# Optimization experiments

Hardware: AMD Instinct MI355X
Metric: run time of the kernel (lower is better)

Reference implementation:

```python
import jax, jax.numpy as jnp
import numpy as np

B, S, DIM = 1, 2048, 4096
N_HEADS, N_KV_HEADS = 32, 8
HEAD_DIM = DIM // N_HEADS            # 128
N_REP = N_HEADS // N_KV_HEADS        # 4
Q_SIZE = N_HEADS * HEAD_DIM          # 4096
KV_SIZE = N_KV_HEADS * HEAD_DIM      # 1024


def setup_inputs() -> dict:
    key = jax.random.key(0)
    ks = jax.random.split(key, 5)
    x = jax.random.normal(ks[0], (B, S, DIM), dtype=jnp.float32)
    # RoPE tables: freqs_cis[s, j] = exp(i * s * theta_j), theta_j = 10000^(-2j/head_dim)
    theta = 10000.0 ** (-jnp.arange(0, HEAD_DIM, 2, dtype=jnp.float32) / HEAD_DIM)
    ang = jnp.arange(S, dtype=jnp.float32)[:, None] * theta[None, :]  # [S, HEAD_DIM//2]
    freqs_cos = jnp.cos(ang)
    freqs_sin = jnp.sin(ang)
    # causal additive mask [1,1,S,S]
    causal = jnp.tril(jnp.ones((S, S), dtype=bool))
    mask = jnp.where(causal, 0.0, -1e9).astype(jnp.float32)[None, None]
    wqkv = jax.random.normal(ks[1], (Q_SIZE + 2 * KV_SIZE, DIM), dtype=jnp.float32) * (DIM ** -0.5)
    wo = jax.random.normal(ks[2], (DIM, Q_SIZE), dtype=jnp.float32) * (Q_SIZE ** -0.5)
    return {"x": x, "freqs_cos": freqs_cos, "freqs_sin": freqs_sin, "mask": mask,
            "wqkv": wqkv, "wo": wo}


def _apply_rope(t, cos, sin):
    # t: [B, S, H, D]; cos/sin: [S, D//2]  (complex multiply on (even, odd) pairs)
    b, s, h, d = t.shape
    tp = t.reshape(b, s, h, d // 2, 2)
    t0, t1 = tp[..., 0], tp[..., 1]
    c = cos[None, :, None, :]
    sn = sin[None, :, None, :]
    out = jnp.stack([t0 * c - t1 * sn, t0 * sn + t1 * c], axis=-1)
    return out.reshape(b, s, h, d)


def reference(x, freqs_cos, freqs_sin, mask, wqkv, wo):
    bsz, seqlen, _ = x.shape
    qkv = jnp.einsum('bsd,od->bso', x, wqkv)  # fused QKV projection
    xq = qkv[..., :Q_SIZE].reshape(bsz, seqlen, N_HEADS, HEAD_DIM)
    xk = qkv[..., Q_SIZE:Q_SIZE + KV_SIZE].reshape(bsz, seqlen, N_KV_HEADS, HEAD_DIM)
    xv = qkv[..., Q_SIZE + KV_SIZE:].reshape(bsz, seqlen, N_KV_HEADS, HEAD_DIM)
    # rotary embedding on q, k
    xq = _apply_rope(xq, freqs_cos, freqs_sin)
    xk = _apply_rope(xk, freqs_cos, freqs_sin)
    # cache insertion (prefill: cache == current k/v), layout [B, KVH, S, D]
    cache_k = jnp.swapaxes(xk, 1, 2)
    cache_v = jnp.swapaxes(xv, 1, 2)
    # GQA repeat_kv -> [B, H, S, D]
    keys = jnp.repeat(cache_k, N_REP, axis=1)
    values = jnp.repeat(cache_v, N_REP, axis=1)
    # scores: einsum 'ijkl,ikml->ikjm' with xq [b,s,h,d], keys [b,h,t,d] -> [b,h,s,t]
    scores = jnp.einsum('bshd,bhtd->bhst', xq, keys) / jnp.sqrt(jnp.float32(HEAD_DIM))
    scores = scores + mask
    scores = jax.nn.softmax(scores.astype(jnp.float32), axis=-1).astype(xq.dtype)
    out = jnp.einsum('bhst,bhtd->bhsd', scores, values)  # [B, H, S, D]
    out = jnp.swapaxes(out, 1, 2).reshape(bsz, seqlen, Q_SIZE)
    return jnp.einsum('bso,do->bsd', out, wo)
```

## Files before the change

kernel.cpp:

```cpp
#include <hip/hip_runtime.h>
#include <hip/hip_bf16.h>
#include <cstdint>
#include <cstddef>


typedef __attribute__((ext_vector_type(4)))  float    f32x4;
typedef __attribute__((ext_vector_type(16))) float    f32x16;
typedef __attribute__((ext_vector_type(8)))  __bf16   bf16x8;
typedef __attribute__((ext_vector_type(4)))  __bf16   bf16x4;
typedef __attribute__((ext_vector_type(2)))  __bf16   bf16x2;
typedef __attribute__((ext_vector_type(4)))  uint32_t u32x4;

typedef const __attribute__((address_space(1))) void* gaddr_t;
typedef __attribute__((address_space(3))) void*       laddr_t;

#define S_LEN   2048
#define DIM_    4096
#define NHEADS  32
#define NKV     8
#define HD      128
#define QKV_LD  6144
#define KOFF    4096
#define VOFF    5120

#define EXP2F(x) __builtin_amdgcn_exp2f(x)

#define N4_X  2097152
#define N4_W  6291456
#define N4_O  4194304
__global__ void cvt3(const float* __restrict__ x, __bf16* __restrict__ xb,
                     const float* __restrict__ wq, __bf16* __restrict__ wqb,
                     const float* __restrict__ wo, __bf16* __restrict__ wob) {
  int idx = blockIdx.x * blockDim.x + threadIdx.x;
  int stride = gridDim.x * blockDim.x;
  for (int i = idx; i < N4_X + N4_W + N4_O; i += stride) {
    const float* src; __bf16* dst; int k;
    if (i < N4_X)            { src = x;  dst = xb;  k = i; }
    else if (i < N4_X + N4_W){ src = wq; dst = wqb; k = i - N4_X; }
    else                     { src = wo; dst = wob; k = i - N4_X - N4_W; }
    float4 v = reinterpret_cast<const float4*>(src)[k];
    bf16x4 o;
    o[0] = (__bf16)v.x; o[1] = (__bf16)v.y; o[2] = (__bf16)v.z; o[3] = (__bf16)v.w;
    reinterpret_cast<bf16x4*>(dst)[k] = o;
  }
}

__global__ void rope_kernel(__bf16* __restrict__ qkv, const float* __restrict__ fc,
                            const float* __restrict__ fs) {
  int tid = blockIdx.x * 256 + threadIdx.x;
  int i = tid & 63;
  int t = tid >> 6;
  int h = t % 40;
  int s = t / 40;
  int col = (h < NHEADS) ? (h * HD + 2 * i) : (KOFF + (h - NHEADS) * HD + 2 * i);
  size_t off = (size_t)s * QKV_LD + col;
  float c = fc[s * 64 + i], sn = fs[s * 64 + i];
  bf16x2 v = *reinterpret_cast<bf16x2*>(&qkv[off]);
  float t0 = (float)v[0], t1 = (float)v[1];
  bf16x2 o;
  o[0] = (__bf16)(t0 * c - t1 * sn);
  o[1] = (__bf16)(t0 * sn + t1 * c);
  *reinterpret_cast<bf16x2*>(&qkv[off]) = o;
}

__device__ __forceinline__ void stg64(const __bf16* __restrict__ P, int ld, int row0,
                                      int kt, char* dst, int tid) {
  int r = tid >> 3, g = tid & 7;
  int row = row0 + r;
  const __bf16* src = P + (size_t)row * ld + kt * 64 + ((g ^ (row & 7)) * 8);
  __builtin_amdgcn_global_load_lds((gaddr_t)src,
      (laddr_t)(dst + (tid & ~63) * 16), 16, 0, 0);
}

template <int QM, int QN, bool RA, bool RB, int VW>
__device__ __forceinline__ void g1_phase(const __bf16* __restrict__ Ab,
                                         const __bf16* __restrict__ Bb,
                                         f32x4 (&acc)[8][4],
                                         bf16x8 (&afr)[4][2], bf16x8 (&bfr)[2][2],
                                         int wm, int wn, int l15, int hi, int tid,
                                         const __bf16* __restrict__ SP, int sld,
                                         int srow, int skt, char* sdst, bool doSt) {
  if constexpr (RA) {
#pragma unroll
    for (int fm = 0; fm < 4; ++fm) {
      int R = wm * 128 + QM * 64 + fm * 16 + l15;
#pragma unroll
      for (int kk = 0; kk < 2; ++kk)
        afr[fm][kk] = *reinterpret_cast<const bf16x8*>(
            (const char*)Ab + R * 128 + (((kk * 4 + hi) ^ (R & 7)) * 16));
    }
  }
  if constexpr (RB) {
#pragma unroll
    for (int fn = 0; fn < 2; ++fn) {
      int R = wn * 64 + QN * 32 + fn * 16 + l15;
#pragma unroll
      for (int kk = 0; kk < 2; ++kk)
        bfr[fn][kk] = *reinterpret_cast<const bf16x8*>(
            (const char*)Bb + R * 128 + (((kk * 4 + hi) ^ (R & 7)) * 16));
    }
  }
  if (doSt) {
    stg64(SP, sld, srow, skt, sdst, tid);
    stg64(SP, sld, srow + 64, skt, sdst + 8192, tid);
  }
  __builtin_amdgcn_s_barrier();
  asm volatile("s_waitcnt lgkmcnt(0)" ::: "memory");
  __builtin_amdgcn_sched_barrier(0);
  __builtin_amdgcn_s_setprio(1);
#pragma unroll
  for (int kk = 0; kk < 2; ++kk)
#pragma unroll
    for (int fm = 0; fm < 4; ++fm)
#pragma unroll
      for (int fn = 0; fn < 2; ++fn)
        acc[QM * 4 + fm][QN * 2 + fn] = __builtin_amdgcn_mfma_f32_16x16x32_bf16(
            afr[fm][kk], bfr[fn][kk], acc[QM * 4 + fm][QN * 2 + fn], 0, 0, 0);
  __builtin_amdgcn_s_setprio(0);
  if constexpr (VW == 4) asm volatile("s_waitcnt vmcnt(4)" ::: "memory");
  if constexpr (VW == 0) asm volatile("s_waitcnt vmcnt(0)" ::: "memory");
  __builtin_amdgcn_s_barrier();
}

__global__ __launch_bounds__(512) void g1_8p(const __bf16* __restrict__ A,
                                             const __bf16* __restrict__ B,
                                             __bf16* __restrict__ C, int K,
                                             int lda, int ldb, int ldc) {
  __shared__ __align__(16) __bf16 As[2][256 * 64];
  __shared__ __align__(16) __bf16 Bs[2][256 * 64];
  const int tid = threadIdx.x;
  const int l15 = tid & 15, hi = (tid >> 4) & 3, w = tid >> 6;
  const int wm = w >> 2, wn = w & 3;
  const int bid = blockIdx.x, xcd = bid & 7, lid = bid >> 3;
  const int m0 = (lid % 8) * 256;
  const int n0 = (xcd * 3 + lid / 8) * 256;

  f32x4 acc[8][4] = {};
  bf16x8 afr[4][2], bfr[2][2];
  char* A0 = (char*)As[0]; char* A1 = (char*)As[1];
  char* B0 = (char*)Bs[0]; char* B1 = (char*)Bs[1];

  stg64(A, lda, m0,       0, A0,         tid); stg64(A, lda, m0 + 64,  0, A0 + 8192,  tid);
  stg64(B, ldb, n0,       0, B0,         tid); stg64(B, ldb, n0 + 64,  0, B0 + 8192,  tid);
  stg64(A, lda, m0 + 128, 0, A0 + 16384, tid); stg64(A, lda, m0 + 192, 0, A0 + 24576, tid);
  stg64(B, ldb, n0 + 128, 0, B0 + 16384, tid); stg64(B, ldb, n0 + 192, 0, B0 + 24576, tid);
  stg64(A, lda, m0,       1, A1,         tid); stg64(A, lda, m0 + 64,  1, A1 + 8192,  tid);
  stg64(B, ldb, n0 + 128, 1, B1 + 16384, tid); stg64(B, ldb, n0 + 192, 1, B1 + 24576, tid);
  asm volatile("s_waitcnt vmcnt(4)" ::: "memory");
  __builtin_amdgcn_s_barrier();

  const int nt = K >> 6;
  for (int it = 0; it < nt; it += 2) {
    const bool sB = (it + 2 < nt), sC = (it + 3 < nt);
    const bool last = !sB;
    const __bf16* Ab0 = As[0]; const __bf16* Bb0 = Bs[0];
    const __bf16* Ab1 = As[1]; const __bf16* Bb1 = Bs[1];
    g1_phase<0, 0, true,  true, -1>(Ab0, Bb0, acc, afr, bfr, wm, wn, l15, hi, tid,
                                    A, lda, m0 + 128, it + 1, A1 + 16384, true);
    g1_phase<0, 1, false, true, -1>(Ab0, Bb0, acc, afr, bfr, wm, wn, l15, hi, tid,
                                    B, ldb, n0, it + 1, B1, true);
    g1_phase<1, 1, true, false, -1>(Ab0, Bb0, acc, afr, bfr, wm, wn, l15, hi, tid,
                                    A, lda, m0, it + 2, A0, sB);
    if (last)
      g1_phase<1, 0, false, true, 0>(Ab0, Bb0, acc, afr, bfr, wm, wn, l15, hi, tid,
                                     B, ldb, n0 + 128, it + 2, B0 + 16384, sB);
    else
      g1_phase<1, 0, false, true, 4>(Ab0, Bb0, acc, afr, bfr, wm, wn, l15, hi, tid,
                                     B, ldb, n0 + 128, it + 2, B0 + 16384, sB);
    g1_phase<0, 0, true,  true, -1>(Ab1, Bb1, acc, afr, bfr, wm, wn, l15, hi, tid,
                                    A, lda, m0 + 128, it + 2, A0 + 16384, sB);
    g1_phase<0, 1, false, true, -1>(Ab1, Bb1, acc, afr, bfr, wm, wn, l15, hi, tid,
                                    B, ldb, n0, it + 2, B0, sB);
    g1_phase<1, 1, true, false, -1>(Ab1, Bb1, acc, afr, bfr, wm, wn, l15, hi, tid,
                                    A, lda, m0, it + 3, A1, sC);
    if (last)
      g1_phase<1, 0, false, true, 0>(Ab1, Bb1, acc, afr, bfr, wm, wn, l15, hi, tid,
                                     B, ldb, n0 + 128, it + 3, B1 + 16384, sC);
    else
      g1_phase<1, 0, false, true, 4>(Ab1, Bb1, acc, afr, bfr, wm, wn, l15, hi, tid,
                                     B, ldb, n0 + 128, it + 3, B1 + 16384, sC);
  }

#pragma unroll
  for (int qm = 0; qm < 2; ++qm)
#pragma unroll
    for (int fm = 0; fm < 4; ++fm)
#pragma unroll
      for (int qn = 0; qn < 2; ++qn)
#pragma unroll
        for (int fn = 0; fn < 2; ++fn)
#pragma unroll
          for (int j = 0; j < 4; ++j) {
            int row = m0 + wm * 128 + qm * 64 + fm * 16 + hi * 4 + j;
            int col = n0 + wn * 64 + qn * 32 + fn * 16 + l15;
            C[(size_t)row * ldc + col] = (__bf16)acc[qm * 4 + fm][qn * 2 + fn][j];
          }
}

template <int QM, int QN, bool RA, bool RB, int VW, int NS>
__device__ __forceinline__ void g2_phase(const __bf16* __restrict__ Ab,
                                         const __bf16* __restrict__ Bb,
                                         f32x4 (&acc)[4][4],
                                         bf16x8 (&afr)[2][2], bf16x8 (&bfr)[2][2],
                                         int wm, int wn, int l15, int hi, int tid,
                                         const __bf16* __restrict__ SP, int sld,
                                         int srow, int skt, char* sdst, bool doSt) {
  if constexpr (RA) {
#pragma unroll
    for (int fm = 0; fm < 2; ++fm) {
      int R = wm * 64 + QM * 32 + fm * 16 + l15;
#pragma unroll
      for (int kk = 0; kk < 2; ++kk)
        afr[fm][kk] = *reinterpret_cast<const bf16x8*>(
            (const char*)Ab + R * 128 + (((kk * 4 + hi) ^ (R & 7)) * 16));
    }
  }
  if constexpr (RB) {
#pragma unroll
    for (int fn = 0; fn < 2; ++fn) {
      int R = wn * 64 + QN * 32 + fn * 16 + l15;
#pragma unroll
      for (int kk = 0; kk < 2; ++kk)
        bfr[fn][kk] = *reinterpret_cast<const bf16x8*>(
            (const char*)Bb + R * 128 + (((kk * 4 + hi) ^ (R & 7)) * 16));
    }
  }
  if (doSt) {
#pragma unroll
    for (int s = 0; s < NS; ++s)
      stg64(SP, sld, srow + s * 64, skt, sdst + s * 8192, tid);
  }
  __builtin_amdgcn_s_barrier();
  asm volatile("s_waitcnt lgkmcnt(0)" ::: "memory");
  __builtin_amdgcn_sched_barrier(0);
  __builtin_amdgcn_s_setprio(1);
#pragma unroll
  for (int kk = 0; kk < 2; ++kk)
#pragma unroll
    for (int fm = 0; fm < 2; ++fm)
#pragma unroll
      for (int fn = 0; fn < 2; ++fn)
        acc[QM * 2 + fm][QN * 2 + fn] = __builtin_amdgcn_mfma_f32_16x16x32_bf16(
            afr[fm][kk], bfr[fn][kk], acc[QM * 2 + fm][QN * 2 + fn], 0, 0, 0);
  __builtin_amdgcn_s_setprio(0);
  if constexpr (VW == 3) asm volatile("s_waitcnt vmcnt(3)" ::: "memory");
  if constexpr (VW == 0) asm volatile("s_waitcnt vmcnt(0)" ::: "memory");
  __builtin_amdgcn_s_barrier();
}

__global__ __launch_bounds__(512) void g2_8p(const __bf16* __restrict__ A,
                                             const __bf16* __restrict__ B,
                                             float* __restrict__ C, int K,
                                             int lda, int ldb, int ldc) {
  __shared__ __align__(16) __bf16 As[2][128 * 64];
  __shared__ __align__(16) __bf16 Bs[2][256 * 64];
  const int tid = threadIdx.x;
  const int l15 = tid & 15, hi = (tid >> 4) & 3, w = tid >> 6;
  const int wm = w >> 2, wn = w & 3;
  const int bid = blockIdx.x, xcd = bid & 7, lid = bid >> 3;
  const int m0 = (lid % 16) * 128;
  const int n0 = (xcd * 2 + lid / 16) * 256;

  f32x4 acc[4][4] = {};
  bf16x8 afr[2][2], bfr[2][2];
  char* A0 = (char*)As[0]; char* A1 = (char*)As[1];
  char* B0 = (char*)Bs[0]; char* B1 = (char*)Bs[1];

  stg64(A, lda, m0,       0, A0,         tid);
  stg64(B, ldb, n0,       0, B0,         tid); stg64(B, ldb, n0 + 64,  0, B0 + 8192,  tid);
  stg64(A, lda, m0 + 64,  0, A0 + 8192,  tid);
  stg64(B, ldb, n0 + 128, 0, B0 + 16384, tid); stg64(B, ldb, n0 + 192, 0, B0 + 24576, tid);
  stg64(A, lda, m0,       1, A1,         tid);
  stg64(B, ldb, n0 + 128, 1, B1 + 16384, tid); stg64(B, ldb, n0 + 192, 1, B1 + 24576, tid);
  asm volatile("s_waitcnt vmcnt(3)" ::: "memory");
  __builtin_amdgcn_s_barrier();

  const int nt = K >> 6;
  for (int it = 0; it < nt; it += 2) {
    const bool sB = (it + 2 < nt), sC = (it + 3 < nt);
    const bool last = !sB;
    const __bf16* Ab0 = As[0]; const __bf16* Bb0 = Bs[0];
    const __bf16* Ab1 = As[1]; const __bf16* Bb1 = Bs[1];
    g2_phase<0, 0, true,  true, -1, 1>(Ab0, Bb0, acc, afr, bfr, wm, wn, l15, hi, tid,
                                       A, lda, m0 + 64, it + 1, A1 + 8192, true);
    g2_phase<0, 1, false, true, -1, 2>(Ab0, Bb0, acc, afr, bfr, wm, wn, l15, hi, tid,
                                       B, ldb, n0, it + 1, B1, true);
    g2_phase<1, 1, true, false, -1, 1>(Ab0, Bb0, acc, afr, bfr, wm, wn, l15, hi, tid,
                                       A, lda, m0, it + 2, A0, sB);
    if (last)
      g2_phase<1, 0, false, true, 0, 2>(Ab0, Bb0, acc, afr, bfr, wm, wn, l15, hi, tid,
                                        B, ldb, n0 + 128, it + 2, B0 + 16384, sB);
    else
      g2_phase<1, 0, false, true, 3, 2>(Ab0, Bb0, acc, afr, bfr, wm, wn, l15, hi, tid,
                                        B, ldb, n0 + 128, it + 2, B0 + 16384, sB);
    g2_phase<0, 0, true,  true, -1, 1>(Ab1, Bb1, acc, afr, bfr, wm, wn, l15, hi, tid,
                                       A, lda, m0 + 64, it + 2, A0 + 8192, sB);
    g2_phase<0, 1, false, true, -1, 2>(Ab1, Bb1, acc, afr, bfr, wm, wn, l15, hi, tid,
                                       B, ldb, n0, it + 2, B0, sB);
    g2_phase<1, 1, true, false, -1, 1>(Ab1, Bb1, acc, afr, bfr, wm, wn, l15, hi, tid,
                                       A, lda, m0, it + 3, A1, sC);
    if (last)
      g2_phase<1, 0, false, true, 0, 2>(Ab1, Bb1, acc, afr, bfr, wm, wn, l15, hi, tid,
                                        B, ldb, n0 + 128, it + 3, B1 + 16384, sC);
    else
      g2_phase<1, 0, false, true, 3, 2>(Ab1, Bb1, acc, afr, bfr, wm, wn, l15, hi, tid,
                                        B, ldb, n0 + 128, it + 3, B1 + 16384, sC);
  }

#pragma unroll
  for (int qm = 0; qm < 2; ++qm)
#pragma unroll
    for (int fm = 0; fm < 2; ++fm)
#pragma unroll
      for (int qn = 0; qn < 2; ++qn)
#pragma unroll
        for (int fn = 0; fn < 2; ++fn)
#pragma unroll
          for (int j = 0; j < 4; ++j) {
            int row = m0 + wm * 64 + qm * 32 + fm * 16 + hi * 4 + j;
            int col = n0 + wn * 64 + qn * 32 + fn * 16 + l15;
            C[(size_t)row * ldc + col] = acc[qm * 2 + fm][qn * 2 + fn][j];
          }
}

__device__ inline uint32_t pack2(float a, float b) {
  bf16x2 t; t[0] = (__bf16)a; t[1] = (__bf16)b;
  return __builtin_bit_cast(uint32_t, t);
}

__global__ __launch_bounds__(256, 2) void attn_kernel(const __bf16* __restrict__ qkv,
                                                      __bf16* __restrict__ out) {
  __shared__ __align__(16) __bf16 Ks[2][64 * 128];
  __shared__ __align__(16) __bf16 Vt[2][128][66];
  const int tid = threadIdx.x;
  const int lane = tid & 63, l31 = lane & 31, hi = lane >> 5, wq = tid >> 6;
  const int head = blockIdx.x & 31;
  const int g = blockIdx.x >> 5;
  const int qt = (g < 8) ? (15 - g) : (g - 8);
  const int q0 = qt * 128;
  const int nt = 2 * qt + 2;
  const int kvh = head >> 2;
  const float sc2 = 0.08838834764831845f * 1.44269504089f;
  const int qr = q0 + wq * 32 + l31;

  bf16x8 vr[2][2];

  auto stage_k = [&](int tt, int buf) {
#pragma unroll
    for (int i = 0; i < 4; ++i) {
      int c = i * 256 + tid;
      int r = c >> 4, gg = c & 15;
      const __bf16* gk = qkv + (size_t)(tt * 64 + r) * QKV_LD + KOFF + kvh * HD + ((gg ^ (r & 7)) * 8);
      __builtin_amdgcn_global_load_lds((gaddr_t)gk,
          (laddr_t)((char*)Ks[buf] + (tid & ~63) * 16 + i * 4096), 16, 0, 0);
    }
  };
  auto load_v = [&](int tt) {
#pragma unroll
    for (int i = 0; i < 2; ++i) {
      int task = i * 256 + tid;
      int p = task >> 4, cg = task & 15;
      const __bf16* vp = qkv + (size_t)(tt * 64 + 2 * p) * QKV_LD + VOFF + kvh * HD + cg * 8;
      vr[i][0] = *reinterpret_cast<const bf16x8*>(vp);
      vr[i][1] = *reinterpret_cast<const bf16x8*>(vp + QKV_LD);
    }
  };
  auto write_v = [&](int buf) {
#pragma unroll
    for (int i = 0; i < 2; ++i) {
      int task = i * 256 + tid;
      int p = task >> 4, cg = task & 15;
#pragma unroll
      for (int e = 0; e < 8; ++e) {
        bf16x2 pkv; pkv[0] = vr[i][0][e]; pkv[1] = vr[i][1][e];
        *reinterpret_cast<bf16x2*>(&Vt[buf][cg * 8 + e][2 * p]) = pkv;
      }
    }
  };

  bf16x8 qf[8];
  {
    const __bf16* qp = qkv + (size_t)qr * QKV_LD + head * HD + hi * 8;
#pragma unroll
    for (int ks = 0; ks < 8; ++ks) qf[ks] = *reinterpret_cast<const bf16x8*>(qp + ks * 16);
  }
  f32x16 o[4] = {};
  float m_run = -3e38f, l_run = 0.f;

  stage_k(0, 0); load_v(0); write_v(0);

  for (int t = 0; t < nt; ++t) {
    const int cur = t & 1;
    __syncthreads();
    if (t + 1 < nt) { stage_k(t + 1, 1 - cur); load_v(t + 1); }

    f32x16 st[2];
    __builtin_amdgcn_s_setprio(1);
#pragma unroll
    for (int sub = 0; sub < 2; ++sub) {
      f32x16 acc = {};
      int r = sub * 32 + l31;
#pragma unroll
      for (int ks = 0; ks < 8; ++ks) {
        int gg = (ks * 2 + hi) ^ (r & 7);
        bf16x8 kf = *reinterpret_cast<const bf16x8*>((char*)Ks[cur] + r * 256 + gg * 16);
        acc = __builtin_amdgcn_mfma_f32_32x32x16_bf16(kf, qf[ks], acc, 0, 0, 0);
      }
      st[sub] = acc;
    }
    __builtin_amdgcn_s_setprio(0);
    if (t >= nt - 2) {
      const int kv0 = t * 64;
#pragma unroll
      for (int sub = 0; sub < 2; ++sub)
#pragma unroll
        for (int e = 0; e < 16; ++e) {
          int kvg = kv0 + sub * 32 + (e & 3) + 8 * (e >> 2) + 4 * hi;
          if (kvg > qr) st[sub][e] = -1e30f;
        }
    }
    float pm = st[0][0];
#pragma unroll
    for (int e = 1; e < 16; ++e) pm = fmaxf(pm, st[0][e]);
#pragma unroll
    for (int e = 0; e < 16; ++e) pm = fmaxf(pm, st[1][e]);
    pm = fmaxf(pm, __shfl_xor(pm, 32));
    pm *= sc2;
    if (!__all(pm - m_run <= 8.f)) {
      float mn = fmaxf(m_run, pm);
      float fsc = EXP2F(m_run - mn);
      m_run = mn;
      l_run *= fsc;
#pragma unroll
      for (int dt = 0; dt < 4; ++dt)
#pragma unroll
        for (int e = 0; e < 16; ++e) o[dt][e] *= fsc;
    }
    float rs = 0.f;
#pragma unroll
    for (int sub = 0; sub < 2; ++sub)
#pragma unroll
      for (int e = 0; e < 16; ++e) {
        float p = EXP2F(__builtin_fmaf(st[sub][e], sc2, -m_run));
        st[sub][e] = p;
        rs += p;
      }
    rs += __shfl_xor(rs, 32);
    l_run += rs;

    uint32_t pk[16];
#pragma unroll
    for (int sub = 0; sub < 2; ++sub)
#pragma unroll
      for (int i = 0; i < 8; ++i)
        pk[sub * 8 + i] = pack2(st[sub][2 * i], st[sub][2 * i + 1]);
    uint32_t rv[8];
#pragma unroll
    for (int m = 0; m < 8; ++m) {
      int base = 4 * (m >> 1) + (m & 1);
      uint32_t snd = hi ? pk[base] : pk[base + 2];
      rv[m] = __shfl_xor(snd, 32);
    }
    bf16x8 pf[4];
#pragma unroll
    for (int tt = 0; tt < 4; ++tt) {
      u32x4 wv;
      wv[0] = hi ? rv[2 * tt]     : pk[4 * tt];
      wv[1] = hi ? rv[2 * tt + 1] : pk[4 * tt + 1];
      wv[2] = hi ? pk[4 * tt + 2] : rv[2 * tt];
      wv[3] = hi ? pk[4 * tt + 3] : rv[2 * tt + 1];
      pf[tt] = __builtin_bit_cast(bf16x8, wv);
    }
    __builtin_amdgcn_s_setprio(1);
#pragma unroll
    for (int dt = 0; dt < 4; ++dt) {
      int dr = dt * 32 + l31;
#pragma unroll
      for (int tt = 0; tt < 4; ++tt) {
        bf16x8 vf = *reinterpret_cast<const bf16x8*>((char*)&Vt[cur][0][0] + dr * 132 + tt * 32 + hi * 16);
        o[dt] = __builtin_amdgcn_mfma_f32_32x32x16_bf16(vf, pf[tt], o[dt], 0, 0, 0);
      }
    }
    __builtin_amdgcn_s_setprio(0);
    if (t + 1 < nt) write_v(1 - cur);
  }

  float inv = 1.f / l_run;
  __bf16* scr = &Ks[0][0] + wq * 1280;
  const int qq = lane >> 1, part = lane & 1;
#pragma unroll
  for (int dt = 0; dt < 4; ++dt) {
    __syncthreads();
#pragma unroll
    for (int i = 0; i < 8; ++i) {
      int d0 = (2 * i & 3) + 8 * (i >> 1) + 4 * hi;
      bf16x2 prr;
      prr[0] = (__bf16)(o[dt][2 * i] * inv);
      prr[1] = (__bf16)(o[dt][2 * i + 1] * inv);
      *reinterpret_cast<bf16x2*>(scr + l31 * 40 + d0) = prr;
    }
    __syncthreads();
    bf16x8 r0 = *reinterpret_cast<const bf16x8*>(scr + qq * 40 + part * 16);
    bf16x8 r1 = *reinterpret_cast<const bf16x8*>(scr + qq * 40 + part * 16 + 8);
    __bf16* op = out + (size_t)(q0 + wq * 32 + qq) * DIM_ + head * HD + dt * 32 + part * 16;
    *reinterpret_cast<bf16x8*>(op) = r0;
    *reinterpret_cast<bf16x8*>(op + 8) = r1;
  }
}

extern "C" void kernel_launch(void* const* d_in, const int* in_sizes, int n_in,
                              void* d_out, int out_size, void* d_ws, size_t ws_size,
                              hipStream_t stream) {
  (void)in_sizes; (void)n_in; (void)out_size; (void)ws_size;
  const float* x    = (const float*)d_in[0];
  const float* fc   = (const float*)d_in[1];
  const float* fs   = (const float*)d_in[2];
  const float* wqkv = (const float*)d_in[4];
  const float* wo   = (const float*)d_in[5];
  float* out = (float*)d_out;

  char* ws = (char*)d_ws;
  __bf16* xb    = (__bf16*)(ws);
  __bf16* wqkvb = (__bf16*)(ws + 16777216);
  __bf16* wob   = (__bf16*)(ws + 67108864);
  __bf16* qkv   = (__bf16*)(ws + 100663296);
  __bf16* attnO = xb;

  cvt3<<<2048, 256, 0, stream>>>(x, xb, wqkv, wqkvb, wo, wob);

  g1_8p<<<192, 512, 0, stream>>>(xb, wqkvb, qkv, DIM_, DIM_, DIM_, QKV_LD);

  rope_kernel<<<(S_LEN * 40 * 64) / 256, 256, 0, stream>>>(qkv, fc, fs);

  attn_kernel<<<512, 256, 0, stream>>>(qkv, attnO);

  g2_8p<<<256, 512, 0, stream>>>(attnO, wob, out, DIM_, DIM_, DIM_, DIM_);
}
```

Baseline: 321.4 us.

## Retile QKV GEMM to 128x384 blocks for 256-CTA grid

Changes the QKV projection GEMM tile from 256x256 to 128x384, launching 256 workgroups instead of 192 so every one of the 256 CUs gets a block. Per-wave fragments become 2x3 MFMA tiles, and LDS staging is split as one A chunk and three B chunks per phase, with matching prefetch offsets. This trades lower arithmetic intensity per block (more global/L2 traffic for A) for better CU occupancy and wave balance.

```diff
diff --git a/kernel.cpp b/kernel.cpp
--- a/kernel.cpp
+++ b/kernel.cpp
@@ -72,18 +72,18 @@
       (laddr_t)(dst + (tid & ~63) * 16), 16, 0, 0);
 }
 
-template <int QM, int QN, bool RA, bool RB, int VW>
+template <int QM, int QN, bool RA, bool RB, int VW, int NS>
 __device__ __forceinline__ void g1_phase(const __bf16* __restrict__ Ab,
                                          const __bf16* __restrict__ Bb,
-                                         f32x4 (&acc)[8][4],
-                                         bf16x8 (&afr)[4][2], bf16x8 (&bfr)[2][2],
+                                         f32x4 (&acc)[4][6],
+                                         bf16x8 (&afr)[2][2], bf16x8 (&bfr)[3][2],
                                          int wm, int wn, int l15, int hi, int tid,
                                          const __bf16* __restrict__ SP, int sld,
                                          int srow, int skt, char* sdst, bool doSt) {
   if constexpr (RA) {
 #pragma unroll
-    for (int fm = 0; fm < 4; ++fm) {
-      int R = wm * 128 + QM * 64 + fm * 16 + l15;
+    for (int fm = 0; fm < 2; ++fm) {
+      int R = wm * 64 + QM * 32 + fm * 16 + l15;
 #pragma unroll
       for (int kk = 0; kk < 2; ++kk)
         afr[fm][kk] = *reinterpret_cast<const bf16x8*>(
@@ -92,8 +92,8 @@
   }
   if constexpr (RB) {
 #pragma unroll
-    for (int fn = 0; fn < 2; ++fn) {
-      int R = wn * 64 + QN * 32 + fn * 16 + l15;
+    for (int fn = 0; fn < 3; ++fn) {
+      int R = wn * 96 + QN * 48 + fn * 16 + l15;
 #pragma unroll
       for (int kk = 0; kk < 2; ++kk)
         bfr[fn][kk] = *reinterpret_cast<const bf16x8*>(
@@ -101,8 +101,9 @@
     }
   }
   if (doSt) {
-    stg64(SP, sld, srow, skt, sdst, tid);
-    stg64(SP, sld, srow + 64, skt, sdst + 8192, tid);
+#pragma unroll
+    for (int s = 0; s < NS; ++s)
+      stg64(SP, sld, srow + s * 64, skt, sdst + s * 8192, tid);
   }
   __builtin_amdgcn_s_barrier();
   asm volatile("s_waitcnt lgkmcnt(0)" ::: "memory");
@@ -111,11 +112,11 @@
 #pragma unroll
   for (int kk = 0; kk < 2; ++kk)
 #pragma unroll
-    for (int fm = 0; fm < 4; ++fm)
-#pragma unroll
-      for (int fn = 0; fn < 2; ++fn)
-        acc[QM * 4 + fm][QN * 2 + fn] = __builtin_amdgcn_mfma_f32_16x16x32_bf16(
-            afr[fm][kk], bfr[fn][kk], acc[QM * 4 + fm][QN * 2 + fn], 0, 0, 0);
+    for (int fm = 0; fm < 2; ++fm)
+#pragma unroll
+      for (int fn = 0; fn < 3; ++fn)
+        acc[QM * 2 + fm][QN * 3 + fn] = __builtin_amdgcn_mfma_f32_16x16x32_bf16(
+            afr[fm][kk], bfr[fn][kk], acc[QM * 2 + fm][QN * 3 + fn], 0, 0, 0);
   __builtin_amdgcn_s_setprio(0);
   if constexpr (VW == 4) asm volatile("s_waitcnt vmcnt(4)" ::: "memory");
   if constexpr (VW == 0) asm volatile("s_waitcnt vmcnt(0)" ::: "memory");
@@ -126,26 +127,32 @@
                                              const __bf16* __restrict__ B,
                                              __bf16* __restrict__ C, int K,
                                              int lda, int ldb, int ldc) {
-  __shared__ __align__(16) __bf16 As[2][256 * 64];
-  __shared__ __align__(16) __bf16 Bs[2][256 * 64];
+  __shared__ __align__(16) __bf16 As[2][128 * 64];
+  __shared__ __align__(16) __bf16 Bs[2][384 * 64];
   const int tid = threadIdx.x;
   const int l15 = tid & 15, hi = (tid >> 4) & 3, w = tid >> 6;
   const int wm = w >> 2, wn = w & 3;
   const int bid = blockIdx.x, xcd = bid & 7, lid = bid >> 3;
-  const int m0 = (lid % 8) * 256;
-  const int n0 = (xcd * 3 + lid / 8) * 256;
-
-  f32x4 acc[8][4] = {};
-  bf16x8 afr[4][2], bfr[2][2];
+  const int m0 = ((xcd >> 1) * 4 + (lid & 3)) * 128;
+  const int n0 = ((xcd & 1) * 8 + (lid >> 2)) * 384;
+
+  f32x4 acc[4][6] = {};
+  bf16x8 afr[2][2], bfr[3][2];
   char* A0 = (char*)As[0]; char* A1 = (char*)As[1];
   char* B0 = (char*)Bs[0]; char* B1 = (char*)Bs[1];
-
-  stg64(A, lda, m0,       0, A0,         tid); stg64(A, lda, m0 + 64,  0, A0 + 8192,  tid);
-  stg64(B, ldb, n0,       0, B0,         tid); stg64(B, ldb, n0 + 64,  0, B0 + 8192,  tid);
-  stg64(A, lda, m0 + 128, 0, A0 + 16384, tid); stg64(A, lda, m0 + 192, 0, A0 + 24576, tid);
-  stg64(B, ldb, n0 + 128, 0, B0 + 16384, tid); stg64(B, ldb, n0 + 192, 0, B0 + 24576, tid);
-  stg64(A, lda, m0,       1, A1,         tid); stg64(A, lda, m0 + 64,  1, A1 + 8192,  tid);
-  stg64(B, ldb, n0 + 128, 1, B1 + 16384, tid); stg64(B, ldb, n0 + 192, 1, B1 + 24576, tid);
+  const int Bh = 192 * 128;
+
+  stg64(A, lda, m0,       0, A0,         tid);
+  stg64(B, ldb, n0,       0, B0,         tid); stg64(B, ldb, n0 + 64,  0, B0 + 8192, tid);
+  stg64(B, ldb, n0 + 128, 0, B0 + 16384, tid);
+  stg64(A, lda, m0 + 64,  0, A0 + 8192,  tid);
+  stg64(B, ldb, n0 + 192, 0, B0 + Bh,         tid);
+  stg64(B, ldb, n0 + 256, 0, B0 + Bh + 8192,  tid);
+  stg64(B, ldb, n0 + 320, 0, B0 + Bh + 16384, tid);
+  stg64(A, lda, m0,       1, A1,         tid);
+  stg64(B, ldb, n0 + 192, 1, B1 + Bh,         tid);
+  stg64(B, ldb, n0 + 256, 1, B1 + Bh + 8192,  tid);
+  stg64(B, ldb, n0 + 320, 1, B1 + Bh + 16384, tid);
   asm volatile("s_waitcnt vmcnt(4)" ::: "memory");
   __builtin_amdgcn_s_barrier();
 
@@ -155,45 +162,45 @@
     const bool last = !sB;
     const __bf16* Ab0 = As[0]; const __bf16* Bb0 = Bs[0];
     const __bf16* Ab1 = As[1]; const __bf16* Bb1 = Bs[1];
-    g1_phase<0, 0, true,  true, -1>(Ab0, Bb0, acc, afr, bfr, wm, wn, l15, hi, tid,
-                                    A, lda, m0 + 128, it + 1, A1 + 16384, true);
-    g1_phase<0, 1, false, true, -1>(Ab0, Bb0, acc, afr, bfr, wm, wn, l15, hi, tid,
-                                    B, ldb, n0, it + 1, B1, true);
-    g1_phase<1, 1, true, false, -1>(Ab0, Bb0, acc, afr, bfr, wm, wn, l15, hi, tid,
-                                    A, lda, m0, it + 2, A0, sB);
+    g1_phase<0, 0, true,  true, -1, 1>(Ab0, Bb0, acc, afr, bfr, wm, wn, l15, hi, tid,
+                                       A, lda, m0 + 64, it + 1, A1 + 8192, true);
+    g1_phase<0, 1, false, true, -1, 3>(Ab0, Bb0, acc, afr, bfr, wm, wn, l15, hi, tid,
+                                       B, ldb, n0, it + 1, B1, true);
+    g1_phase<1, 1, true, false, -1, 1>(Ab0, Bb0, acc, afr, bfr, wm, wn, l15, hi, tid,
+                                       A, lda, m0, it + 2, A0, sB);
     if (last)
-      g1_phase<1, 0, false, true, 0>(Ab0, Bb0, acc, afr, bfr, wm, wn, l15, hi, tid,
-                                     B, ldb, n0 + 128, it + 2, B0 + 16384, sB);
+      g1_phase<1, 0, false, true, 0, 3>(Ab0, Bb0, acc, afr, bfr, wm, wn, l15, hi, tid,
+                                        B, ldb, n0 + 192, it + 2, B0 + Bh, sB);
     else
-      g1_phase<1, 0, false, true, 4>(Ab0, Bb0, acc, afr, bfr, wm, wn, l15, hi, tid,
-                                     B, ldb, n0 + 128, it + 2, B0 + 16384, sB);
-    g1_phase<0, 0, true,  true, -1>(Ab1, Bb1, acc, afr, bfr, wm, wn, l15, hi, tid,
-                                    A, lda, m0 + 128, it + 2, A0 + 16384, sB);
-    g1_phase<0, 1, false, true, -1>(Ab1, Bb1, acc, afr, bfr, wm, wn, l15, hi, tid,
-                                    B, ldb, n0, it + 2, B0, sB);
-    g1_phase<1, 1, true, false, -1>(Ab1, Bb1, acc, afr, bfr, wm, wn, l15, hi, tid,
-                                    A, lda, m0, it + 3, A1, sC);
+      g1_phase<1, 0, false, true, 4, 3>(Ab0, Bb0, acc, afr, bfr, wm, wn, l15, hi, tid,
+                                        B, ldb, n0 + 192, it + 2, B0 + Bh, sB);
+    g1_phase<0, 0, true,  true, -1, 1>(Ab1, Bb1, acc, afr, bfr, wm, wn, l15, hi, tid,
+                                       A, lda, m0 + 64, it + 2, A0 + 8192, sB);
+    g1_phase<0, 1, false, true, -1, 3>(Ab1, Bb1, acc, afr, bfr, wm, wn, l15, hi, tid,
+                                       B, ldb, n0, it + 2, B0, sB);
+    g1_phase<1, 1, true, false, -1, 1>(Ab1, Bb1, acc, afr, bfr, wm, wn, l15, hi, tid,
+                                       A, lda, m0, it + 3, A1, sC);
     if (last)
-      g1_phase<1, 0, false, true, 0>(Ab1, Bb1, acc, afr, bfr, wm, wn, l15, hi, tid,
-                                     B, ldb, n0 + 128, it + 3, B1 + 16384, sC);
+      g1_phase<1, 0, false, true, 0, 3>(Ab1, Bb1, acc, afr, bfr, wm, wn, l15, hi, tid,
+                                        B, ldb, n0 + 192, it + 3, B1 + Bh, sC);
     else
-      g1_phase<1, 0, false, true, 4>(Ab1, Bb1, acc, afr, bfr, wm, wn, l15, hi, tid,
-                                     B, ldb, n0 + 128, it + 3, B1 + 16384, sC);
+      g1_phase<1, 0, false, true, 4, 3>(Ab1, Bb1, acc, afr, bfr, wm, wn, l15, hi, tid,
+                                        B, ldb, n0 + 192, it + 3, B1 + Bh, sC);
   }
 
 #pragma unroll
   for (int qm = 0; qm < 2; ++qm)
 #pragma unroll
-    for (int fm = 0; fm < 4; ++fm)
+    for (int fm = 0; fm < 2; ++fm)
 #pragma unroll
       for (int qn = 0; qn < 2; ++qn)
 #pragma unroll
-        for (int fn = 0; fn < 2; ++fn)
+        for (int fn = 0; fn < 3; ++fn)
 #pragma unroll
           for (int j = 0; j < 4; ++j) {
-            int row = m0 + wm * 128 + qm * 64 + fm * 16 + hi * 4 + j;
-            int col = n0 + wn * 64 + qn * 32 + fn * 16 + l15;
-            C[(size_t)row * ldc + col] = (__bf16)acc[qm * 4 + fm][qn * 2 + fn][j];
+            int row = m0 + wm * 64 + qm * 32 + fm * 16 + hi * 4 + j;
+            int col = n0 + wn * 96 + qn * 48 + fn * 16 + l15;
+            C[(size_t)row * ldc + col] = (__bf16)acc[qm * 2 + fm][qn * 3 + fn][j];
           }
 }
 
@@ -528,7 +535,7 @@
 
   cvt3<<<2048, 256, 0, stream>>>(x, xb, wqkv, wqkvb, wo, wob);
 
-  g1_8p<<<192, 512, 0, stream>>>(xb, wqkvb, qkv, DIM_, DIM_, DIM_, QKV_LD);
+  g1_8p<<<256, 512, 0, stream>>>(xb, wqkvb, qkv, DIM_, DIM_, DIM_, QKV_LD);
 
   rope_kernel<<<(S_LEN * 40 * 64) / 256, 256, 0, stream>>>(qkv, fc, fs);
 
```

Result: no change. 317.9 us (-1.1%).
